# Kernel tuning notes

Measured on AMD Instinct MI355X. Metric: run time of the kernel, lower is better.

The kernel has to match this reference:

```python
import jax, jax.numpy as jnp
import numpy as np

H, C = 8, 32          # heads, out_channels per head (H*C = 256)
D = H * C
NEG_SLOPE = 0.2
SELF_LOOP_TYPE = 6    # num_edge_types - 1
EPS_LN = 1e-5
EPS_BN = 1e-5


def _gat_layer(x, src, dst, ea, et, Ws, Wd, a_s, a_d, We, ae, te, Wo, bo, b, lg, lb):
    N = x.shape[0]
    xs = (x @ Ws).reshape(N, H, C)   # lin_src -> x_j features
    xd = (x @ Wd).reshape(N, H, C)   # lin_dst -> x_i features
    # per-node attention logits (gathered per edge): alpha = <x_i, att_src> + <x_j, att_dst>
    a_i = jnp.einsum('nhc,hc->nh', xd, a_s)  # paired with x_i (dst)
    a_j = jnp.einsum('nhc,hc->nh', xs, a_d)  # paired with x_j (src)
    alpha = a_i[dst] + a_j[src]                                  # [E, H]
    ef = (ea @ We).reshape(-1, H, C)                              # lin_edge
    alpha = alpha + jnp.einsum('ehc,hc->eh', ef, ae)
    tf = te[et].reshape(-1, H, C)                                 # edge_type_emb
    alpha = alpha + jnp.einsum('ehc,hc->eh', tf, ae)
    alpha = jnp.where(alpha >= 0, alpha, NEG_SLOPE * alpha)       # leaky_relu
    # segment softmax over destination nodes (every node has a self loop)
    m = jax.ops.segment_max(alpha, dst, num_segments=N)
    e = jnp.exp(alpha - m[dst])
    s = jax.ops.segment_sum(e, dst, num_segments=N)
    alpha = e / (s[dst] + 1e-16)                                  # [E, H]
    # dropout is identity in eval mode
    msg = xs[src] * alpha[:, :, None]                             # [E, H, C]
    out = jax.ops.segment_sum(msg, dst, num_segments=N).reshape(N, D)
    out = out @ Wo + bo + b                                       # lin_out + bias
    mu = out.mean(-1, keepdims=True)
    var = out.var(-1, keepdims=True)
    out = (out - mu) / jnp.sqrt(var + EPS_LN) * lg + lb           # layer norm
    return out + x                                                # in_channels == H*C residual


def _bn_relu(x, g, bvec, relu=True):
    mu = x.mean(0)
    var = x.var(0)
    x = (x - mu) / jnp.sqrt(var + EPS_BN) * g + bvec
    return jnp.maximum(x, 0.0) if relu else x


def _forward(x, edge_index, edge_attr, edge_types,
             Ws1, Wd1, as1, ad1, We1, ae1, te1, Wo1, bo1, b1, lg1, lb1,
             Ws2, Wd2, as2, ad2, We2, ae2, te2, Wo2, bo2, b2, lg2, lb2,
             bng1, bnb1, bng2, bnb2):
    N = x.shape[0]
    loops = jnp.arange(N, dtype=edge_index.dtype)
    src = jnp.concatenate([edge_index[0], loops])
    dst = jnp.concatenate([edge_index[1], loops])
    ea = jnp.concatenate([edge_attr, jnp.ones((N, edge_attr.shape[1]), edge_attr.dtype)])
    et = jnp.concatenate([edge_types, jnp.full((N,), SELF_LOOP_TYPE, edge_types.dtype)])
    residual = x  # in_channels == out_channels -> identity projection
    out = _gat_layer(x, src, dst, ea, et, Ws1, Wd1, as1, ad1, We1, ae1, te1, Wo1, bo1, b1, lg1, lb1)
    out = _bn_relu(out, bng1, bnb1, relu=True)   # dropout identity in eval
    out = _gat_layer(out, src, dst, ea, et, Ws2, Wd2, as2, ad2, We2, ae2, te2, Wo2, bo2, b2, lg2, lb2)
    out = _bn_relu(out, bng2, bnb2, relu=False)
    return jnp.maximum(out + residual, 0.0)


def setup_inputs() -> dict:
    key = jax.random.key(0)
    ks = jax.random.split(key, 32)
    N, E, EDIM, NTYPES = 20000, 320000, 16, 7
    d = {}
    d['x'] = jax.random.normal(ks[0], (N, D), jnp.float32)
    d['edge_index'] = jax.random.randint(ks[1], (2, E), 0, N, jnp.int64)
    d['edge_attr'] = jax.random.normal(ks[2], (E, EDIM), jnp.float32)
    d['edge_types'] = jax.random.randint(ks[3], (E,), 0, NTYPES, jnp.int64)
    def glorot(k, shape):
        fan = shape[-2] + shape[-1] if len(shape) >= 2 else shape[-1] + 1
        return jax.random.uniform(k, shape, jnp.float32, -1.0, 1.0) * np.sqrt(6.0 / fan)
    i = 4
    for L in ('1', '2'):
        d['Ws' + L] = glorot(ks[i], (D, D)); i += 1
        d['Wd' + L] = glorot(ks[i], (D, D)); i += 1
        d['as' + L] = glorot(ks[i], (H, C)); i += 1
        d['ad' + L] = glorot(ks[i], (H, C)); i += 1
        d['We' + L] = glorot(ks[i], (EDIM, D)); i += 1
        d['ae' + L] = glorot(ks[i], (H, C)); i += 1
        d['te' + L] = glorot(ks[i], (NTYPES, D)); i += 1
        d['Wo' + L] = glorot(ks[i], (D, D)); i += 1
        d['bo' + L] = jnp.zeros((D,), jnp.float32)
        d['b' + L] = jnp.zeros((D,), jnp.float32)
        d['lg' + L] = jnp.ones((D,), jnp.float32)
        d['lb' + L] = jnp.zeros((D,), jnp.float32)
    d['bng1'] = jnp.ones((D,), jnp.float32); d['bnb1'] = jnp.zeros((D,), jnp.float32)
    d['bng2'] = jnp.ones((D,), jnp.float32); d['bnb2'] = jnp.zeros((D,), jnp.float32)
    return d


def reference(x, edge_index, edge_attr, edge_types,
              Ws1, Wd1, as1, ad1, We1, ae1, te1, Wo1, bo1, b1, lg1, lb1,
              Ws2, Wd2, as2, ad2, We2, ae2, te2, Wo2, bo2, b2, lg2, lb2,
              bng1, bnb1, bng2, bnb2):
    return _forward(x, edge_index, edge_attr, edge_types,
                    Ws1, Wd1, as1, ad1, We1, ae1, te1, Wo1, bo1, b1, lg1, lb1,
                    Ws2, Wd2, as2, ad2, We2, ae2, te2, Wo2, bo2, b2, lg2, lb2,
                    bng1, bnb1, bng2, bnb2)
```

## Files before the change

### kernel.cpp

```cpp
#include <hip/hip_runtime.h>

#define DD 256
#define HH 8
#define CC 32

typedef __attribute__((ext_vector_type(8))) short short8;
typedef __attribute__((ext_vector_type(4))) float f32x4;

static __device__ __forceinline__ unsigned short f2b(float f){
  unsigned u = __float_as_uint(f);
  u = u + 0x7FFFu + ((u >> 16) & 1u);
  return (unsigned short)(u >> 16);
}
static __device__ __forceinline__ float b2f(unsigned short s){
  return __uint_as_float(((unsigned)s) << 16);
}

static __device__ __forceinline__ void gload16(const void* g, void* l){
  using gpt = const __attribute__((address_space(1))) unsigned int*;
  using lpt = __attribute__((address_space(3))) unsigned int*;
  __builtin_amdgcn_global_load_lds((gpt)(unsigned long long)g, (lpt)(unsigned long long)l, 16, 0, 0);
}

__global__ void k_zero_i(int* p, int n){ int i=blockIdx.x*blockDim.x+threadIdx.x; if(i<n) p[i]=0; }

__global__ void k_count(const int* __restrict__ dstE, int E, int N, int* cnt){
  int e=blockIdx.x*blockDim.x+threadIdx.x;
  if(e<E+N){ int d=(e<E)? dstE[e] : (e-E); atomicAdd(&cnt[d],1); }
}

__global__ __launch_bounds__(1024) void k_scan(const int* __restrict__ cnt, int N, int* row_off, int* cursor){
  __shared__ int part[1024];
  int t=threadIdx.x;
  int chunk=(N+1023)>>10;
  int s=0;
  for(int j=0;j<chunk;j++){ int i=t*chunk+j; if(i<N) s+=cnt[i]; }
  part[t]=s; __syncthreads();
  for(int off=1; off<1024; off<<=1){
    int v=(t>=off)? part[t-off]:0;
    __syncthreads();
    part[t]+=v;
    __syncthreads();
  }
  int run=(t==0)?0:part[t-1];
  for(int j=0;j<chunk;j++){ int i=t*chunk+j; if(i<N){ row_off[i]=run; cursor[i]=run; run+=cnt[i]; } }
  if(t==1023) row_off[N]=part[1023];
}

__global__ void k_fill(const int* __restrict__ srcE, const int* __restrict__ dstE, int E, int N,
                       int* cursor, int* epos, int* esrc){
  int e=blockIdx.x*blockDim.x+threadIdx.x;
  if(e>=E+N) return;
  int s,d;
  if(e<E){ s=srcE[e]; d=dstE[e]; } else { s=e-E; d=s; }
  int pos=atomicAdd(&cursor[d],1);
  epos[e]=pos; esrc[pos]=s;
}

__global__ void k_cvt_wT4(const float* __restrict__ W0, const float* __restrict__ W1,
                          const float* __restrict__ W2, const float* __restrict__ W3,
                          unsigned short* __restrict__ T0, unsigned short* __restrict__ T1,
                          unsigned short* __restrict__ T2, unsigned short* __restrict__ T3){
  int m=blockIdx.y, c=blockIdx.x, k=threadIdx.x;
  const float* W = (m==0)?W0:(m==1)?W1:(m==2)?W2:W3;
  unsigned short* T = (m==0)?T0:(m==1)?T1:(m==2)?T2:T3;
  T[(size_t)c*DD+k] = f2b(W[(size_t)k*DD+c]);
}

__global__ void k_pre2(const float* __restrict__ Wd1, const float* __restrict__ as1,
                       const float* __restrict__ We1, const float* __restrict__ ae1,
                       const float* __restrict__ te1,
                       const float* __restrict__ Wd2, const float* __restrict__ as2,
                       const float* __restrict__ We2, const float* __restrict__ ae2,
                       const float* __restrict__ te2,
                       float* wd_as1, float* v_e1, float* t_a1,
                       float* wd_as2, float* v_e2, float* t_a2){
  int L=blockIdx.x;
  const float* Wd=L?Wd2:Wd1; const float* as_=L?as2:as1;
  const float* We=L?We2:We1; const float* ae=L?ae2:ae1; const float* te=L?te2:te1;
  float* wd_as=L?wd_as2:wd_as1; float* v_e=L?v_e2:v_e1; float* t_a=L?t_a2:t_a1;
  int t=threadIdx.x;
  for(int idx=t; idx<DD*HH; idx+=256){
    int k=idx>>3, h=idx&7;
    const float* w=&Wd[k*DD+h*CC]; const float* a=&as_[h*CC];
    float s=0;
    #pragma unroll
    for(int c=0;c<CC;c++) s+=w[c]*a[c];
    wd_as[idx]=s;
  }
  for(int idx=t; idx<16*HH; idx+=256){
    int k=idx>>3, h=idx&7;
    const float* w=&We[k*DD+h*CC]; const float* a=&ae[h*CC];
    float s=0;
    #pragma unroll
    for(int c=0;c<CC;c++) s+=w[c]*a[c];
    v_e[idx]=s;
  }
  for(int idx=t; idx<7*HH; idx+=256){
    int k=idx>>3, h=idx&7;
    const float* w=&te[k*DD+h*CC]; const float* a=&ae[h*CC];
    float s=0;
    #pragma unroll
    for(int c=0;c<CC;c++) s+=w[c]*a[c];
    t_a[idx]=s;
  }
}

#define NB_BA 1024
__global__ __launch_bounds__(256) void k_cvt_x2(const float* __restrict__ xin, const float* __restrict__ wd_as,
                         unsigned short* __restrict__ xb, float* __restrict__ a_i, int N){
  int b=blockIdx.x, tid=threadIdx.x, wv=tid>>6, l=tid&63;
  int c0=4*l;
  float wa[4][8];
  #pragma unroll
  for(int j=0;j<4;j++)
    #pragma unroll
    for(int h=0;h<8;h++) wa[j][h]=wd_as[(c0+j)*8+h];
  for(int n=b*4+wv; n<N; n+=NB_BA*4){
    float4 v=*(const float4*)&xin[(size_t)n*DD+c0];
    ushort4 xo; xo.x=f2b(v.x); xo.y=f2b(v.y); xo.z=f2b(v.z); xo.w=f2b(v.w);
    *(ushort4*)&xb[(size_t)n*DD+c0]=xo;
    float ai[8];
    #pragma unroll
    for(int h=0;h<8;h++) ai[h]=v.x*wa[0][h]+v.y*wa[1][h]+v.z*wa[2][h]+v.w*wa[3][h];
    #pragma unroll
    for(int off=1;off<64;off<<=1){
      #pragma unroll
      for(int h=0;h<8;h++) ai[h]+=__shfl_xor(ai[h],off);
    }
    if(l==0){
      float4 A; A.x=ai[0];A.y=ai[1];A.z=ai[2];A.w=ai[3];
      float4 B; B.x=ai[4];B.y=ai[5];B.z=ai[6];B.w=ai[7];
      *(float4*)&a_i[(size_t)n*HH]=A;
      *(float4*)&a_i[(size_t)n*HH+4]=B;
    }
  }
}

template<bool AJ>
__global__ __launch_bounds__(256) void k_gemm1(const unsigned short* __restrict__ A,
                                               const unsigned short* __restrict__ Bt,
                                               const float* __restrict__ ad, float* __restrict__ a_j,
                                               unsigned short* __restrict__ Cout, int N){
  __shared__ char lds[2*12288];
  int tid=threadIdx.x;
  int w=tid>>6, l=tid&63;
  int row0=blockIdx.y*64, col0=blockIdx.x*128;

  int lr=l>>2;
  int kc=(l&3)^((l>>3)&3);
  const unsigned short* ga  = &A [(size_t)(row0+16*w+lr)*DD + kc*8];
  const unsigned short* gb0 = &Bt[(size_t)(col0+32*w+lr)*DD + kc*8];
  const unsigned short* gb1 = &Bt[(size_t)(col0+32*w+16+lr)*DD + kc*8];
  int laoff =      w*1024;
  int lboff0=4096+(32*w)*64;
  int lboff1=4096+(32*w+16)*64;

  int x15=l&15;
  int lp=x15*64 + ((l>>4)^((x15>>1)&3))*16;

  f32x4 acc[4][2];
  #pragma unroll
  for(int i=0;i<4;i++){ acc[i][0]=(f32x4)0.f; acc[i][1]=(f32x4)0.f; }

  gload16(ga,  lds+laoff);
  gload16(gb0, lds+lboff0);
  gload16(gb1, lds+lboff1);
  __syncthreads();
  int cur=0;
  for(int kt=0;kt<DD;kt+=32){
    int nxt=cur^1;
    if(kt+32<DD){
      gload16(ga +kt+32, lds+nxt*12288+laoff);
      gload16(gb0+kt+32, lds+nxt*12288+lboff0);
      gload16(gb1+kt+32, lds+nxt*12288+lboff1);
    }
    char* base=lds+cur*12288;
    short8 af[4], bf[2];
    #pragma unroll
    for(int mf=0;mf<4;mf++) af[mf]=*(short8*)(base + mf*1024 + lp);
    #pragma unroll
    for(int nf=0;nf<2;nf++) bf[nf]=*(short8*)(base + 4096 + (32*w+16*nf)*64 + lp);
    #pragma unroll
    for(int mf=0;mf<4;mf++)
      #pragma unroll
      for(int nf=0;nf<2;nf++)
        acc[mf][nf]=__builtin_amdgcn_mfma_f32_16x16x32_bf16(af[mf],bf[nf],acc[mf][nf],0,0,0);
    __syncthreads();
    cur=nxt;
  }

  int lcol=x15, lrow4=(l>>4)*4;
  float ad0=0.f, ad1=0.f;
  if(AJ){ ad0=ad[col0+32*w+lcol]; ad1=ad[col0+32*w+16+lcol]; }
  int head=(col0>>5)+w;
  #pragma unroll
  for(int mf=0;mf<4;mf++){
    #pragma unroll
    for(int nf=0;nf<2;nf++){
      int col=col0 + 32*w + 16*nf + lcol;
      #pragma unroll
      for(int rr=0;rr<4;rr++){
        int row=row0 + 16*mf + lrow4 + rr;
        if(row<N) Cout[(size_t)row*DD+col]=f2b(acc[mf][nf][rr]);
      }
    }
    if(AJ){
      #pragma unroll
      for(int rr=0;rr<4;rr++){
        float t=acc[mf][0][rr]*ad0 + acc[mf][1][rr]*ad1;
        t+=__shfl_xor(t,1); t+=__shfl_xor(t,2);
        t+=__shfl_xor(t,4); t+=__shfl_xor(t,8);
        int row=row0 + 16*mf + lrow4 + rr;
        if(x15==0 && row<N) a_j[(size_t)row*HH+head]=t;
      }
    }
  }
}

__global__ __launch_bounds__(256) void k_gemm_ln(const unsigned short* __restrict__ A,
                                                 const unsigned short* __restrict__ Bt,
                                                 const float* __restrict__ bo, const float* __restrict__ bvec,
                                                 const float* __restrict__ xin,
                                                 const float* __restrict__ lg, const float* __restrict__ lb,
                                                 float* __restrict__ hout,
                                                 float* __restrict__ psum, float* __restrict__ psq, int N){
  __shared__ char lds[2*18432];
  int tid=threadIdx.x;
  int w=tid>>6, l=tid&63;
  int row0=blockIdx.x*32;

  int lr=l>>2;
  int kc=(l&3)^((l>>3)&3);
  const unsigned short* ga = &A[(size_t)(row0+16*w+lr)*DD + kc*8];
  const unsigned short* gb0=&Bt[(size_t)(64*w   +lr)*DD + kc*8];
  const unsigned short* gb1=&Bt[(size_t)(64*w+16+lr)*DD + kc*8];
  const unsigned short* gb2=&Bt[(size_t)(64*w+32+lr)*DD + kc*8];
  const unsigned short* gb3=&Bt[(size_t)(64*w+48+lr)*DD + kc*8];
  int laoff =      w*1024;
  int lboff0=2048+(64*w   )*64;
  int lboff1=2048+(64*w+16)*64;
  int lboff2=2048+(64*w+32)*64;
  int lboff3=2048+(64*w+48)*64;

  int x15=l&15;
  int lp=x15*64 + ((l>>4)^((x15>>1)&3))*16;

  f32x4 acc[2][4];
  #pragma unroll
  for(int i=0;i<2;i++)
    #pragma unroll
    for(int j=0;j<4;j++) acc[i][j]=(f32x4)0.f;

  if(w<2) gload16(ga, lds+laoff);
  gload16(gb0, lds+lboff0);
  gload16(gb1, lds+lboff1);
  gload16(gb2, lds+lboff2);
  gload16(gb3, lds+lboff3);
  __syncthreads();
  int cur=0;
  for(int kt=0;kt<DD;kt+=32){
    int nxt=cur^1;
    if(kt+32<DD){
      char* nb=lds+nxt*18432;
      if(w<2) gload16(ga+kt+32, nb+laoff);
      gload16(gb0+kt+32, nb+lboff0);
      gload16(gb1+kt+32, nb+lboff1);
      gload16(gb2+kt+32, nb+lboff2);
      gload16(gb3+kt+32, nb+lboff3);
    }
    char* base=lds+cur*18432;
    short8 af[2], bf[4];
    #pragma unroll
    for(int mf=0;mf<2;mf++) af[mf]=*(short8*)(base + mf*1024 + lp);
    #pragma unroll
    for(int nf=0;nf<4;nf++) bf[nf]=*(short8*)(base + 2048 + (64*w+16*nf)*64 + lp);
    #pragma unroll
    for(int mf=0;mf<2;mf++)
      #pragma unroll
      for(int nf=0;nf<4;nf++)
        acc[mf][nf]=__builtin_amdgcn_mfma_f32_16x16x32_bf16(af[mf],bf[nf],acc[mf][nf],0,0,0);
    __syncthreads();
    cur=nxt;
  }

  int lrow4=(l>>4)*4;
  float lgv[4], lbv[4];
  #pragma unroll
  for(int nf=0;nf<4;nf++){
    int col=64*w+16*nf+x15;
    float badd=bo[col]+bvec[col];
    lgv[nf]=lg[col]; lbv[nf]=lb[col];
    #pragma unroll
    for(int mf=0;mf<2;mf++)
      #pragma unroll
      for(int rr=0;rr<4;rr++) acc[mf][nf][rr]+=badd;
  }
  __syncthreads();
  float* rs   =(float*)lds;
  float* rq   =(float*)(lds+512);
  float* mus  =(float*)(lds+1024);
  float* rstds=(float*)(lds+1152);
  #pragma unroll
  for(int mf=0;mf<2;mf++){
    #pragma unroll
    for(int rr=0;rr<4;rr++){
      float t=acc[mf][0][rr]+acc[mf][1][rr]+acc[mf][2][rr]+acc[mf][3][rr];
      float q=acc[mf][0][rr]*acc[mf][0][rr]+acc[mf][1][rr]*acc[mf][1][rr]
             +acc[mf][2][rr]*acc[mf][2][rr]+acc[mf][3][rr]*acc[mf][3][rr];
      t+=__shfl_xor(t,1); q+=__shfl_xor(q,1);
      t+=__shfl_xor(t,2); q+=__shfl_xor(q,2);
      t+=__shfl_xor(t,4); q+=__shfl_xor(q,4);
      t+=__shfl_xor(t,8); q+=__shfl_xor(q,8);
      if(x15==0){
        int row=16*mf+lrow4+rr;
        rs[w*32+row]=t; rq[w*32+row]=q;
      }
    }
  }
  __syncthreads();
  if(tid<32){
    float S=rs[tid]+rs[32+tid]+rs[64+tid]+rs[96+tid];
    float Q=rq[tid]+rq[32+tid]+rq[64+tid]+rq[96+tid];
    float mu=S*(1.f/DD);
    float var=Q*(1.f/DD)-mu*mu;
    mus[tid]=mu;
    rstds[tid]=rsqrtf(var+1e-5f);
  }
  __syncthreads();
  float cps[4]={0.f,0.f,0.f,0.f}, cqs[4]={0.f,0.f,0.f,0.f};
  #pragma unroll
  for(int mf=0;mf<2;mf++){
    #pragma unroll
    for(int rr=0;rr<4;rr++){
      int row=16*mf+lrow4+rr;
      int grow=row0+row;
      bool ok=(grow<N);
      float mu=mus[row], rstd=rstds[row];
      #pragma unroll
      for(int nf=0;nf<4;nf++){
        int col=64*w+16*nf+x15;
        float h=0.f;
        if(ok){
          h=(acc[mf][nf][rr]-mu)*rstd*lgv[nf]+lbv[nf]+xin[(size_t)grow*DD+col];
          hout[(size_t)grow*DD+col]=h;
        }
        cps[nf]+=h; cqs[nf]+=h*h;
      }
    }
  }
  #pragma unroll
  for(int nf=0;nf<4;nf++){
    cps[nf]+=__shfl_xor(cps[nf],16); cqs[nf]+=__shfl_xor(cqs[nf],16);
    cps[nf]+=__shfl_xor(cps[nf],32); cqs[nf]+=__shfl_xor(cqs[nf],32);
  }
  if(l<16){
    #pragma unroll
    for(int nf=0;nf<4;nf++){
      int col=64*w+16*nf+l;
      psum[(size_t)blockIdx.x*DD+col]=cps[nf];
      psq [(size_t)blockIdx.x*DD+col]=cqs[nf];
    }
  }
}

__global__ void k_edge(const int* __restrict__ srcE, const int* __restrict__ dstE,
                       const float* __restrict__ ea, const int* __restrict__ et,
                       const int* __restrict__ epos,
                       const float* __restrict__ a_i, const float* __restrict__ a_j,
                       const float* __restrict__ v_e, const float* __restrict__ t_a,
                       float* __restrict__ alphaP, int E, int N){
  int e=blockIdx.x*blockDim.x+threadIdx.x;
  if(e>=E+N) return;
  int s,d,ty;
  float eattr[16];
  if(e<E){
    s=srcE[e]; d=dstE[e]; ty=et[e];
    float4 q0=*(const float4*)&ea[(size_t)e*16+0];
    float4 q1=*(const float4*)&ea[(size_t)e*16+4];
    float4 q2=*(const float4*)&ea[(size_t)e*16+8];
    float4 q3=*(const float4*)&ea[(size_t)e*16+12];
    eattr[0]=q0.x;eattr[1]=q0.y;eattr[2]=q0.z;eattr[3]=q0.w;
    eattr[4]=q1.x;eattr[5]=q1.y;eattr[6]=q1.z;eattr[7]=q1.w;
    eattr[8]=q2.x;eattr[9]=q2.y;eattr[10]=q2.z;eattr[11]=q2.w;
    eattr[12]=q3.x;eattr[13]=q3.y;eattr[14]=q3.z;eattr[15]=q3.w;
  }else{
    s=e-E; d=s; ty=6;
    #pragma unroll
    for(int k=0;k<16;k++) eattr[k]=1.f;
  }
  int pos=epos[e];
  const float* ai=&a_i[(size_t)d*8];
  const float* aj=&a_j[(size_t)s*8];
  #pragma unroll
  for(int h=0;h<8;h++){
    float v=ai[h]+aj[h]+t_a[ty*8+h];
    #pragma unroll
    for(int k=0;k<16;k++) v+=eattr[k]*v_e[k*8+h];
    alphaP[(size_t)pos*8+h] = (v>=0.f)? v : 0.2f*v;
  }
}

__global__ __launch_bounds__(256) void k_agg(const int* __restrict__ row_off,
                      const int* __restrict__ esrc, const float* __restrict__ alphaP,
                      const unsigned short* __restrict__ ysb, unsigned short* __restrict__ aggb, int N){
  int wv=threadIdx.x>>6, l=threadIdx.x&63;
  int n=blockIdx.x*4+wv;
  if(n>=N) return;
  int beg=row_off[n], deg=row_off[n+1]-beg;
  int slotL=l>>3, headL=l&7;
  float mx=-3e38f;
  for(int i=slotL;i<deg;i+=8) mx=fmaxf(mx, alphaP[(size_t)(beg+i)*8+headL]);
  mx=fmaxf(mx,__shfl_xor(mx,8));
  mx=fmaxf(mx,__shfl_xor(mx,16));
  mx=fmaxf(mx,__shfl_xor(mx,32));
  int ghead=l>>3;
  float ssum=0.f, acc0=0.f, acc1=0.f, acc2=0.f, acc3=0.f;
  float a_c; int s_c;
  {
    int i=slotL; bool ok=(i<deg); int ic=ok?i:(deg-1);
    a_c = ok ? alphaP[(size_t)(beg+i)*8+headL] : -3e38f;
    s_c = esrc[beg+ic];
  }
  for(int base=0;base<deg;base+=8){
    float a_n=-3e38f; int s_n=0;
    if(base+8<deg){
      int i=base+8+slotL; bool ok=(i<deg); int ic=ok?i:(deg-1);
      a_n = ok ? alphaP[(size_t)(beg+i)*8+headL] : -3e38f;
      s_n = esrc[beg+ic];
    }
    float wvv=__expf(a_c-mx);
    int cnt=min(8,deg-base);
    #pragma unroll
    for(int u=0;u<8;u++){
      if(u<cnt){
        float wgt=__shfl(wvv,(u<<3)|ghead);
        int   si =__shfl(s_c,(u<<3));
        ssum+=wgt;
        ushort4 y=*(const ushort4*)&ysb[(size_t)si*DD+4*l];
        acc0+=wgt*b2f(y.x); acc1+=wgt*b2f(y.y); acc2+=wgt*b2f(y.z); acc3+=wgt*b2f(y.w);
      }
    }
    a_c=a_n; s_c=s_n;
  }
  float inv=1.f/(ssum+1e-16f);
  ushort4 o;
  o.x=f2b(acc0*inv); o.y=f2b(acc1*inv); o.z=f2b(acc2*inv); o.w=f2b(acc3*inv);
  *(ushort4*)&aggb[(size_t)n*DD+4*l]=o;
}

__global__ __launch_bounds__(256) void k_bnfin(const float* __restrict__ psum, const float* __restrict__ psq,
                        const float* __restrict__ g, const float* __restrict__ b,
                        float* scale, float* shift, int N, int nb){
  __shared__ float rs[256], rq[256];
  int c=blockIdx.x, tid=threadIdx.x;
  float s=0.f,q=0.f;
  for(int i=tid;i<nb;i+=256){ s+=psum[(size_t)i*DD+c]; q+=psq[(size_t)i*DD+c]; }
  rs[tid]=s; rq[tid]=q;
  __syncthreads();
  #pragma unroll
  for(int off=128;off>0;off>>=1){
    if(tid<off){ rs[tid]+=rs[tid+off]; rq[tid]+=rq[tid+off]; }
    __syncthreads();
  }
  if(tid==0){
    float inv=1.f/(float)N;
    float mu=rs[0]*inv;
    float var=rq[0]*inv - mu*mu;
    float sc=g[c]*rsqrtf(var+1e-5f);
    scale[c]=sc;
    shift[c]=b[c]-mu*sc;
  }
}

template<bool RES, bool CVT>
__global__ __launch_bounds__(256) void k_bnapply(const float* __restrict__ hm, const float* __restrict__ scale,
                          const float* __restrict__ shift, const float* __restrict__ res,
                          float* __restrict__ outp, unsigned short* __restrict__ xb,
                          const float* __restrict__ wd_as, float* __restrict__ a_i, int N){
  int b=blockIdx.x, tid=threadIdx.x, wv=tid>>6, l=tid&63;
  int c0=4*l;
  float4 sc=*(const float4*)&scale[c0];
  float4 sh=*(const float4*)&shift[c0];
  float wa[4][8];
  if(CVT){
    #pragma unroll
    for(int j=0;j<4;j++)
      #pragma unroll
      for(int h=0;h<8;h++) wa[j][h]=wd_as[(c0+j)*8+h];
  }
  for(int n=b*4+wv; n<N; n+=NB_BA*4){
    float4 v=*(const float4*)&hm[(size_t)n*DD+c0];
    v.x=v.x*sc.x+sh.x; v.y=v.y*sc.y+sh.y; v.z=v.z*sc.z+sh.z; v.w=v.w*sc.w+sh.w;
    if(RES){
      float4 rr=*(const float4*)&res[(size_t)n*DD+c0];
      v.x+=rr.x; v.y+=rr.y; v.z+=rr.z; v.w+=rr.w;
    }
    v.x=fmaxf(v.x,0.f); v.y=fmaxf(v.y,0.f); v.z=fmaxf(v.z,0.f); v.w=fmaxf(v.w,0.f);
    *(float4*)&outp[(size_t)n*DD+c0]=v;
    if(CVT){
      ushort4 xo; xo.x=f2b(v.x); xo.y=f2b(v.y); xo.z=f2b(v.z); xo.w=f2b(v.w);
      *(ushort4*)&xb[(size_t)n*DD+c0]=xo;
      float ai[8];
      #pragma unroll
      for(int h=0;h<8;h++) ai[h]=v.x*wa[0][h]+v.y*wa[1][h]+v.z*wa[2][h]+v.w*wa[3][h];
      #pragma unroll
      for(int off=1;off<64;off<<=1){
        #pragma unroll
        for(int h=0;h<8;h++) ai[h]+=__shfl_xor(ai[h],off);
      }
      if(l==0){
        float4 A; A.x=ai[0];A.y=ai[1];A.z=ai[2];A.w=ai[3];
        float4 B; B.x=ai[4];B.y=ai[5];B.z=ai[6];B.w=ai[7];
        *(float4*)&a_i[(size_t)n*HH]=A;
        *(float4*)&a_i[(size_t)n*HH+4]=B;
      }
    }
  }
}

extern "C" void kernel_launch(void* const* d_in, const int* in_sizes, int n_in,
                              void* d_out, int out_size, void* d_ws, size_t ws_size,
                              hipStream_t stream) {
  const float* x  = (const float*)d_in[0];
  const int*   ei = (const int*)d_in[1];
  const float* ea = (const float*)d_in[2];
  const int*   et = (const int*)d_in[3];
  int N = in_sizes[0]/DD;
  int E = in_sizes[3];
  int Etot = E+N;
  const int* srcE = ei;
  const int* dstE = ei + E;

  const float* Ws1=(const float*)d_in[4];  const float* Wd1=(const float*)d_in[5];
  const float* as1=(const float*)d_in[6];  const float* ad1=(const float*)d_in[7];
  const float* We1=(const float*)d_in[8];  const float* ae1=(const float*)d_in[9];
  const float* te1=(const float*)d_in[10]; const float* Wo1=(const float*)d_in[11];
  const float* bo1=(const float*)d_in[12]; const float* b1 =(const float*)d_in[13];
  const float* lg1=(const float*)d_in[14]; const float* lb1=(const float*)d_in[15];
  const float* Ws2=(const float*)d_in[16]; const float* Wd2=(const float*)d_in[17];
  const float* as2=(const float*)d_in[18]; const float* ad2=(const float*)d_in[19];
  const float* We2=(const float*)d_in[20]; const float* ae2=(const float*)d_in[21];
  const float* te2=(const float*)d_in[22]; const float* Wo2=(const float*)d_in[23];
  const float* bo2=(const float*)d_in[24]; const float* b2 =(const float*)d_in[25];
  const float* lg2=(const float*)d_in[26]; const float* lb2=(const float*)d_in[27];
  const float* bng1=(const float*)d_in[28]; const float* bnb1=(const float*)d_in[29];
  const float* bng2=(const float*)d_in[30]; const float* bnb2=(const float*)d_in[31];

  char* p=(char*)d_ws;
  auto alloc=[&](size_t bytes)->void*{ void* r=(void*)p; p+=(bytes+255)&~(size_t)255; return r; };
  unsigned short* xb   =(unsigned short*)alloc((size_t)N*DD*2);
  unsigned short* ysb  =(unsigned short*)alloc((size_t)N*DD*2);
  unsigned short* aggb =(unsigned short*)alloc((size_t)N*DD*2);
  float* alphaP=(float*)alloc((size_t)Etot*HH*4);
  float* xout1 =(float*)alloc((size_t)N*DD*4);
  float* a_i   =(float*)alloc((size_t)N*HH*4);
  float* a_j   =(float*)alloc((size_t)N*HH*4);
  float* wd_as1=(float*)alloc(DD*HH*4);
  float* v_e1  =(float*)alloc(16*HH*4);
  float* t_a1  =(float*)alloc(7*HH*4);
  float* wd_as2=(float*)alloc(DD*HH*4);
  float* v_e2  =(float*)alloc(16*HH*4);
  float* t_a2  =(float*)alloc(7*HH*4);
  int nbLN=(N+31)/32;
  float* psum  =(float*)alloc((size_t)nbLN*DD*4);
  float* psq   =(float*)alloc((size_t)nbLN*DD*4);
  float* scl   =(float*)alloc(256*4);
  float* shf   =(float*)alloc(256*4);
  unsigned short* Wsb1T=(unsigned short*)alloc((size_t)DD*DD*2);
  unsigned short* Wob1T=(unsigned short*)alloc((size_t)DD*DD*2);
  unsigned short* Wsb2T=(unsigned short*)alloc((size_t)DD*DD*2);
  unsigned short* Wob2T=(unsigned short*)alloc((size_t)DD*DD*2);
  int* cnt     =(int*)alloc((size_t)N*4);
  int* row_off =(int*)alloc((size_t)(N+1)*4);
  int* cursor  =(int*)alloc((size_t)N*4);
  int* epos    =(int*)alloc((size_t)Etot*4);
  int* esrc    =(int*)alloc((size_t)Etot*4);
  float* hbuf  =(float*)d_out;

  dim3 gg(2,(N+63)/64);
  int aggGrid=(N+3)/4;

  k_zero_i<<<(N+255)/256,256,0,stream>>>(cnt,N);
  k_count<<<(Etot+255)/256,256,0,stream>>>(dstE,E,N,cnt);
  k_scan<<<1,1024,0,stream>>>(cnt,N,row_off,cursor);
  k_fill<<<(Etot+255)/256,256,0,stream>>>(srcE,dstE,E,N,cursor,epos,esrc);
  k_cvt_wT4<<<dim3(DD,4),DD,0,stream>>>(Ws1,Wo1,Ws2,Wo2,Wsb1T,Wob1T,Wsb2T,Wob2T);
  k_pre2<<<2,256,0,stream>>>(Wd1,as1,We1,ae1,te1,Wd2,as2,We2,ae2,te2,
                             wd_as1,v_e1,t_a1,wd_as2,v_e2,t_a2);

  k_cvt_x2<<<NB_BA,256,0,stream>>>(x,wd_as1,xb,a_i,N);
  k_gemm1<true><<<gg,256,0,stream>>>(xb,Wsb1T,ad1,a_j,ysb,N);
  k_edge<<<(Etot+255)/256,256,0,stream>>>(srcE,dstE,ea,et,epos,a_i,a_j,v_e1,t_a1,alphaP,E,N);
  k_agg<<<aggGrid,256,0,stream>>>(row_off,esrc,alphaP,ysb,aggb,N);
  k_gemm_ln<<<nbLN,256,0,stream>>>(aggb,Wob1T,bo1,b1,x,lg1,lb1,hbuf,psum,psq,N);
  k_bnfin<<<DD,256,0,stream>>>(psum,psq,bng1,bnb1,scl,shf,N,nbLN);
  k_bnapply<false,true><<<NB_BA,256,0,stream>>>(hbuf,scl,shf,nullptr,xout1,xb,wd_as2,a_i,N);

  k_gemm1<true><<<gg,256,0,stream>>>(xb,Wsb2T,ad2,a_j,ysb,N);
  k_edge<<<(Etot+255)/256,256,0,stream>>>(srcE,dstE,ea,et,epos,a_i,a_j,v_e2,t_a2,alphaP,E,N);
  k_agg<<<aggGrid,256,0,stream>>>(row_off,esrc,alphaP,ysb,aggb,N);
  k_gemm_ln<<<nbLN,256,0,stream>>>(aggb,Wob2T,bo2,b2,xout1,lg2,lb2,hbuf,psum,psq,N);
  k_bnfin<<<DD,256,0,stream>>>(psum,psq,bng2,bnb2,scl,shf,N,nbLN);
  k_bnapply<true,false><<<NB_BA,256,0,stream>>>(hbuf,scl,shf,x,(float*)d_out,nullptr,nullptr,nullptr,N);
}
```

Measured before the change: 319.0 us.

## Fuse edge-logit computation into aggregation kernel with CSR-permuted edge attributes

The separate per-edge attention-logit kernel is removed. Instead, k_fill permutes edge attributes and types into CSR order once, and k_agg computes the leaky-relu logits on the fly during its max pass, caching them and the source indices in LDS for up to 128 edges per node. This drops two kernel launches and the alphaP round trip through global memory. In exchange each node's logits are recomputed per layer inside the aggregation, the CSR edge-attribute buffer is wider than alphaP (16 floats per edge instead of 8), and high-degree nodes past the cache fall back to recomputing logits per edge in the second pass.

```diff
diff --git a/kernel.cpp b/kernel.cpp
--- a/kernel.cpp
+++ b/kernel.cpp
@@ -3,6 +3,7 @@
 #define DD 256
 #define HH 8
 #define CC 32
+#define DCACHE 128
 
 typedef __attribute__((ext_vector_type(8))) short short8;
 typedef __attribute__((ext_vector_type(4))) float f32x4;
@@ -47,14 +48,28 @@
   if(t==1023) row_off[N]=part[1023];
 }
 
-__global__ void k_fill(const int* __restrict__ srcE, const int* __restrict__ dstE, int E, int N,
-                       int* cursor, int* epos, int* esrc){
+__global__ void k_fill(const int* __restrict__ srcE, const int* __restrict__ dstE,
+                       const float* __restrict__ ea, const int* __restrict__ et,
+                       int E, int N, int* cursor,
+                       int* esrc, int* etP, float* eaP){
   int e=blockIdx.x*blockDim.x+threadIdx.x;
   if(e>=E+N) return;
-  int s,d;
-  if(e<E){ s=srcE[e]; d=dstE[e]; } else { s=e-E; d=s; }
+  int s,d,ty;
+  float4 q0,q1,q2,q3;
+  if(e<E){
+    s=srcE[e]; d=dstE[e]; ty=et[e];
+    q0=*(const float4*)&ea[(size_t)e*16+0];
+    q1=*(const float4*)&ea[(size_t)e*16+4];
+    q2=*(const float4*)&ea[(size_t)e*16+8];
+    q3=*(const float4*)&ea[(size_t)e*16+12];
+  }else{
+    s=e-E; d=s; ty=6;
+    q0=q1=q2=q3=make_float4(1.f,1.f,1.f,1.f);
+  }
   int pos=atomicAdd(&cursor[d],1);
-  epos[e]=pos; esrc[pos]=s;
+  esrc[pos]=s; etP[pos]=ty;
+  float* o=&eaP[(size_t)pos*16];
+  *(float4*)(o+0)=q0; *(float4*)(o+4)=q1; *(float4*)(o+8)=q2; *(float4*)(o+12)=q3;
 }
 
 __global__ void k_cvt_wT4(const float* __restrict__ W0, const float* __restrict__ W1,
@@ -364,84 +379,78 @@
   }
 }
 
-__global__ void k_edge(const int* __restrict__ srcE, const int* __restrict__ dstE,
-                       const float* __restrict__ ea, const int* __restrict__ et,
-                       const int* __restrict__ epos,
-                       const float* __restrict__ a_i, const float* __restrict__ a_j,
-                       const float* __restrict__ v_e, const float* __restrict__ t_a,
-                       float* __restrict__ alphaP, int E, int N){
-  int e=blockIdx.x*blockDim.x+threadIdx.x;
-  if(e>=E+N) return;
-  int s,d,ty;
-  float eattr[16];
-  if(e<E){
-    s=srcE[e]; d=dstE[e]; ty=et[e];
-    float4 q0=*(const float4*)&ea[(size_t)e*16+0];
-    float4 q1=*(const float4*)&ea[(size_t)e*16+4];
-    float4 q2=*(const float4*)&ea[(size_t)e*16+8];
-    float4 q3=*(const float4*)&ea[(size_t)e*16+12];
-    eattr[0]=q0.x;eattr[1]=q0.y;eattr[2]=q0.z;eattr[3]=q0.w;
-    eattr[4]=q1.x;eattr[5]=q1.y;eattr[6]=q1.z;eattr[7]=q1.w;
-    eattr[8]=q2.x;eattr[9]=q2.y;eattr[10]=q2.z;eattr[11]=q2.w;
-    eattr[12]=q3.x;eattr[13]=q3.y;eattr[14]=q3.z;eattr[15]=q3.w;
-  }else{
-    s=e-E; d=s; ty=6;
-    #pragma unroll
-    for(int k=0;k<16;k++) eattr[k]=1.f;
-  }
-  int pos=epos[e];
-  const float* ai=&a_i[(size_t)d*8];
-  const float* aj=&a_j[(size_t)s*8];
-  #pragma unroll
-  for(int h=0;h<8;h++){
-    float v=ai[h]+aj[h]+t_a[ty*8+h];
-    #pragma unroll
-    for(int k=0;k<16;k++) v+=eattr[k]*v_e[k*8+h];
-    alphaP[(size_t)pos*8+h] = (v>=0.f)? v : 0.2f*v;
-  }
-}
-
 __global__ __launch_bounds__(256) void k_agg(const int* __restrict__ row_off,
-                      const int* __restrict__ esrc, const float* __restrict__ alphaP,
+                      const int* __restrict__ esrc, const int* __restrict__ etP,
+                      const float* __restrict__ eaP,
+                      const float* __restrict__ a_i, const float* __restrict__ a_j,
+                      const float* __restrict__ v_e, const float* __restrict__ t_a,
                       const unsigned short* __restrict__ ysb, unsigned short* __restrict__ aggb, int N){
+  __shared__ float cache[4][DCACHE][8];
+  __shared__ int   scache[4][DCACHE];
   int wv=threadIdx.x>>6, l=threadIdx.x&63;
   int n=blockIdx.x*4+wv;
   if(n>=N) return;
   int beg=row_off[n], deg=row_off[n+1]-beg;
   int slotL=l>>3, headL=l&7;
+  float veh[16];
+  #pragma unroll
+  for(int k=0;k<16;k++) veh[k]=v_e[k*8+headL];
+  float aih=a_i[(size_t)n*HH+headL];
   float mx=-3e38f;
-  for(int i=slotL;i<deg;i+=8) mx=fmaxf(mx, alphaP[(size_t)(beg+i)*8+headL]);
+  for(int i=slotL;i<deg;i+=8){
+    size_t pos=(size_t)(beg+i);
+    int src=esrc[pos];
+    int ty=etP[pos];
+    float aj=a_j[(size_t)src*HH+headL];
+    const float* eap=&eaP[pos*16];
+    float4 q0=*(const float4*)(eap+0);
+    float4 q1=*(const float4*)(eap+4);
+    float4 q2=*(const float4*)(eap+8);
+    float4 q3=*(const float4*)(eap+12);
+    float v=aih+aj+t_a[ty*8+headL];
+    v+=q0.x*veh[0]+q0.y*veh[1]+q0.z*veh[2]+q0.w*veh[3];
+    v+=q1.x*veh[4]+q1.y*veh[5]+q1.z*veh[6]+q1.w*veh[7];
+    v+=q2.x*veh[8]+q2.y*veh[9]+q2.z*veh[10]+q2.w*veh[11];
+    v+=q3.x*veh[12]+q3.y*veh[13]+q3.z*veh[14]+q3.w*veh[15];
+    v=(v>=0.f)? v : 0.2f*v;
+    if(i<DCACHE){
+      cache[wv][i][headL]=v;
+      if(headL==0) scache[wv][i]=src;
+    }
+    mx=fmaxf(mx,v);
+  }
   mx=fmaxf(mx,__shfl_xor(mx,8));
   mx=fmaxf(mx,__shfl_xor(mx,16));
   mx=fmaxf(mx,__shfl_xor(mx,32));
   int ghead=l>>3;
+  float m_g=__shfl(mx,ghead);
   float ssum=0.f, acc0=0.f, acc1=0.f, acc2=0.f, acc3=0.f;
-  float a_c; int s_c;
-  {
-    int i=slotL; bool ok=(i<deg); int ic=ok?i:(deg-1);
-    a_c = ok ? alphaP[(size_t)(beg+i)*8+headL] : -3e38f;
-    s_c = esrc[beg+ic];
-  }
   for(int base=0;base<deg;base+=8){
-    float a_n=-3e38f; int s_n=0;
-    if(base+8<deg){
-      int i=base+8+slotL; bool ok=(i<deg); int ic=ok?i:(deg-1);
-      a_n = ok ? alphaP[(size_t)(beg+i)*8+headL] : -3e38f;
-      s_n = esrc[beg+ic];
-    }
-    float wvv=__expf(a_c-mx);
     int cnt=min(8,deg-base);
     #pragma unroll
     for(int u=0;u<8;u++){
       if(u<cnt){
-        float wgt=__shfl(wvv,(u<<3)|ghead);
-        int   si =__shfl(s_c,(u<<3));
+        int i=base+u;
+        float vv; int si;
+        if(i<DCACHE){
+          vv=cache[wv][i][ghead];
+          si=scache[wv][i];
+        }else{
+          size_t pos=(size_t)(beg+i);
+          si=esrc[pos];
+          int ty=etP[pos];
+          float v=a_i[(size_t)n*HH+ghead]+a_j[(size_t)si*HH+ghead]+t_a[ty*8+ghead];
+          const float* eap=&eaP[pos*16];
+          #pragma unroll
+          for(int k=0;k<16;k++) v+=eap[k]*v_e[k*8+ghead];
+          vv=(v>=0.f)? v : 0.2f*v;
+        }
+        float wgt=__expf(vv-m_g);
         ssum+=wgt;
         ushort4 y=*(const ushort4*)&ysb[(size_t)si*DD+4*l];
         acc0+=wgt*b2f(y.x); acc1+=wgt*b2f(y.y); acc2+=wgt*b2f(y.z); acc3+=wgt*b2f(y.w);
       }
     }
-    a_c=a_n; s_c=s_n;
   }
   float inv=1.f/(ssum+1e-16f);
   ushort4 o;
@@ -552,7 +561,8 @@
   unsigned short* xb   =(unsigned short*)alloc((size_t)N*DD*2);
   unsigned short* ysb  =(unsigned short*)alloc((size_t)N*DD*2);
   unsigned short* aggb =(unsigned short*)alloc((size_t)N*DD*2);
-  float* alphaP=(float*)alloc((size_t)Etot*HH*4);
+  float* eaP   =(float*)alloc((size_t)Etot*16*4);
+  int*   etP   =(int*)alloc((size_t)Etot*4);
   float* xout1 =(float*)alloc((size_t)N*DD*4);
   float* a_i   =(float*)alloc((size_t)N*HH*4);
   float* a_j   =(float*)alloc((size_t)N*HH*4);
@@ -574,7 +584,6 @@
   int* cnt     =(int*)alloc((size_t)N*4);
   int* row_off =(int*)alloc((size_t)(N+1)*4);
   int* cursor  =(int*)alloc((size_t)N*4);
-  int* epos    =(int*)alloc((size_t)Etot*4);
   int* esrc    =(int*)alloc((size_t)Etot*4);
   float* hbuf  =(float*)d_out;
 
@@ -584,22 +593,20 @@
   k_zero_i<<<(N+255)/256,256,0,stream>>>(cnt,N);
   k_count<<<(Etot+255)/256,256,0,stream>>>(dstE,E,N,cnt);
   k_scan<<<1,1024,0,stream>>>(cnt,N,row_off,cursor);
-  k_fill<<<(Etot+255)/256,256,0,stream>>>(srcE,dstE,E,N,cursor,epos,esrc);
+  k_fill<<<(Etot+255)/256,256,0,stream>>>(srcE,dstE,ea,et,E,N,cursor,esrc,etP,eaP);
   k_cvt_wT4<<<dim3(DD,4),DD,0,stream>>>(Ws1,Wo1,Ws2,Wo2,Wsb1T,Wob1T,Wsb2T,Wob2T);
   k_pre2<<<2,256,0,stream>>>(Wd1,as1,We1,ae1,te1,Wd2,as2,We2,ae2,te2,
                              wd_as1,v_e1,t_a1,wd_as2,v_e2,t_a2);
 
   k_cvt_x2<<<NB_BA,256,0,stream>>>(x,wd_as1,xb,a_i,N);
   k_gemm1<true><<<gg,256,0,stream>>>(xb,Wsb1T,ad1,a_j,ysb,N);
-  k_edge<<<(Etot+255)/256,256,0,stream>>>(srcE,dstE,ea,et,epos,a_i,a_j,v_e1,t_a1,alphaP,E,N);
-  k_agg<<<aggGrid,256,0,stream>>>(row_off,esrc,alphaP,ysb,aggb,N);
+  k_agg<<<aggGrid,256,0,stream>>>(row_off,esrc,etP,eaP,a_i,a_j,v_e1,t_a1,ysb,aggb,N);
   k_gemm_ln<<<nbLN,256,0,stream>>>(aggb,Wob1T,bo1,b1,x,lg1,lb1,hbuf,psum,psq,N);
   k_bnfin<<<DD,256,0,stream>>>(psum,psq,bng1,bnb1,scl,shf,N,nbLN);
   k_bnapply<false,true><<<NB_BA,256,0,stream>>>(hbuf,scl,shf,nullptr,xout1,xb,wd_as2,a_i,N);
 
   k_gemm1<true><<<gg,256,0,stream>>>(xb,Wsb2T,ad2,a_j,ysb,N);
-  k_edge<<<(Etot+255)/256,256,0,stream>>>(srcE,dstE,ea,et,epos,a_i,a_j,v_e2,t_a2,alphaP,E,N);
-  k_agg<<<aggGrid,256,0,stream>>>(row_off,esrc,alphaP,ysb,aggb,N);
+  k_agg<<<aggGrid,256,0,stream>>>(row_off,esrc,etP,eaP,a_i,a_j,v_e2,t_a2,ysb,aggb,N);
   k_gemm_ln<<<nbLN,256,0,stream>>>(aggb,Wob2T,bo2,b2,xout1,lg2,lb2,hbuf,psum,psq,N);
   k_bnfin<<<DD,256,0,stream>>>(psum,psq,bng2,bnb2,scl,shf,N,nbLN);
   k_bnapply<true,false><<<NB_BA,256,0,stream>>>(hbuf,scl,shf,x,(float*)d_out,nullptr,nullptr,nullptr,N);
```

Result: no change. 318.4 us (-0.2%).
